# Optimization experiments

Hardware: AMD Instinct MI355X
Metric: run time of the kernel (lower is better)

The kernel has to match this reference:

```python
import math
import jax
import jax.numpy as jnp
import numpy as np

B, S, S_IMG, D, H, MAX_SEQ = 8, 1024, 1, 1024, 16, 1024
HD = D // H


def setup_inputs() -> dict:
    key = jax.random.key(0)
    ks = jax.random.split(key, 8)
    w = 0.02  # GPT-2 init scale keeps softmax well-conditioned
    return {
        "hidden_states": jax.random.normal(ks[0], (B, S, D), jnp.float32),
        "attention_mask": jnp.ones((B, 1, 1, S + S_IMG), jnp.float32),
        "image_hidden_states": jax.random.normal(ks[1], (B, S_IMG, D), jnp.float32),
        "Wc_attn": jax.random.normal(ks[2], (D, 3 * D), jnp.float32) * w,  # Conv1D: x @ W + b
        "bc_attn": jnp.zeros((3 * D,), jnp.float32),
        "Wc_proj": jax.random.normal(ks[3], (D, D), jnp.float32) * w,
        "bc_proj": jnp.zeros((D,), jnp.float32),
        "Wuk": jax.random.normal(ks[4], (D, D), jnp.float32) * w,  # nn.Linear weight: x @ W.T
        "Wuv": jax.random.normal(ks[5], (D, D), jnp.float32) * w,
    }


def _split_heads(x):
    b, s, _ = x.shape
    return x.reshape(b, s, H, HD).transpose(0, 2, 1, 3)  # [B,H,S,hd]


def reference(hidden_states, attention_mask, image_hidden_states,
              Wc_attn, bc_attn, Wc_proj, bc_proj, Wuk, Wuv):
    # c_attn (Conv1D): x @ W + b, then split into q,k,v
    qkv = hidden_states @ Wc_attn + bc_attn
    q, k, v = jnp.split(qkv, 3, axis=-1)
    q, k, v = _split_heads(q), _split_heads(k), _split_heads(v)

    # image KV via bias-free Linear layers, appended to text KV (layer_past=None)
    k_img = _split_heads(image_hidden_states @ Wuk.T)
    v_img = _split_heads(image_hidden_states @ Wuv.T)
    k = jnp.concatenate([k, k_img], axis=2)
    v = jnp.concatenate([v, v_img], axis=2)

    Q, K = q.shape[2], k.shape[2]
    scores = jnp.einsum("bhqd,bhkd->bhqk", q, k) / math.sqrt(HD)

    # causal mask: tril(ones(max_seq_len, max_seq_len+1)) sliced to [Q,K]
    causal = jnp.tril(jnp.ones((MAX_SEQ, MAX_SEQ + 1), bool))[None, None, :Q, :K]
    scores = jnp.where(causal, scores, jnp.float32(-1e9))
    scores = jnp.where(attention_mask == 0, jnp.float32(-1e4), scores)

    p_attn = jax.nn.softmax(scores, axis=-1)  # dropout p=0 -> identity
    x = jnp.einsum("bhqk,bhkd->bhqd", p_attn, v)
    x = x.transpose(0, 2, 1, 3).reshape(hidden_states.shape[0], Q, D)
    return x @ Wc_proj + bc_proj
```

## Files before the change

kernel.cpp:

```cpp
#include <hip/hip_runtime.h>


#define DEVINL __device__ __forceinline__

typedef __attribute__((ext_vector_type(8))) short bf16x8;
typedef __attribute__((ext_vector_type(4))) float f32x4;
typedef __attribute__((ext_vector_type(16))) float f32x16;
typedef __attribute__((ext_vector_type(4))) unsigned int u32x4;

DEVINL unsigned short f2bf(float f) {
  unsigned u = __float_as_uint(f);
  u += 0x7fffu + ((u >> 16) & 1u);
  return (unsigned short)(u >> 16);
}

DEVINL void gload_lds16(const void* g, void* l) {
  __builtin_amdgcn_global_load_lds(
      (const __attribute__((address_space(1))) void*)g,
      (__attribute__((address_space(3))) void*)l, 16, 0, 0);
}

#define BARRIER() asm volatile("s_barrier" ::: "memory")

__global__ void cast_f32_bf16(const float* __restrict__ in,
                              unsigned short* __restrict__ out, int n4) {
  int i = blockIdx.x * blockDim.x + threadIdx.x;
  if (i >= n4) return;
  float4 f = ((const float4*)in)[i];
  uint2 o;
  o.x = (unsigned)f2bf(f.x) | ((unsigned)f2bf(f.y) << 16);
  o.y = (unsigned)f2bf(f.z) | ((unsigned)f2bf(f.w) << 16);
  ((uint2*)out)[i] = o;
}

__global__ void transpose_cast(const float* __restrict__ in,
                               unsigned short* __restrict__ out,
                               int rows, int cols) {
  __shared__ unsigned short tile[32][33];
  int bx = blockIdx.x * 32, by = blockIdx.y * 32;
  int tx = threadIdx.x, ty = threadIdx.y;
#pragma unroll
  for (int i = 0; i < 32; i += 8)
    tile[ty + i][tx] = f2bf(in[(size_t)(by + ty + i) * cols + bx + tx]);
  __syncthreads();
#pragma unroll
  for (int i = 0; i < 32; i += 8)
    out[(size_t)(bx + ty + i) * rows + by + tx] = tile[tx][ty + i];
}

DEVINL void stage_tile(const unsigned short* __restrict__ A,
                       const unsigned short* __restrict__ Bt, int m0, int n0,
                       int kt, int buf, int t, int w, unsigned char* lds) {
  const int base = buf * 24576;
#pragma unroll
  for (int i = 0; i < 2; i++) {
    const int idx = i * 256 + t;
    const int r = idx >> 2, p = idx & 3;
    const int c = p ^ ((r >> 1) & 3);
    gload_lds16(A + (size_t)(m0 + r) * 1024 + kt * 32 + c * 8,
                lds + base + (i * 256 + w * 64) * 16);
  }
#pragma unroll
  for (int i = 0; i < 4; i++) {
    const int idx = i * 256 + t;
    const int r = idx >> 2, p = idx & 3;
    const int c = p ^ ((r >> 1) & 3);
    gload_lds16(Bt + (size_t)(n0 + r) * 1024 + kt * 32 + c * 8,
                lds + base + 8192 + (i * 256 + w * 64) * 16);
  }
}

DEVINL bf16x8 readA2(const unsigned char* lds, int buf, int m, int wr, int lr,
                     int lg) {
  const int row = wr * 64 + m * 16 + lr;
  const int off = (lg ^ ((row >> 1) & 3)) << 4;
  return *(const bf16x8*)(lds + buf * 24576 + row * 64 + off);
}
DEVINL bf16x8 readB2(const unsigned char* lds, int buf, int n, int wc, int lr,
                     int lg) {
  const int row = wc * 128 + n * 16 + lr;
  const int off = (lg ^ ((row >> 1) & 3)) << 4;
  return *(const bf16x8*)(lds + buf * 24576 + 8192 + row * 64 + off);
}

DEVINL void gemm_core(const unsigned short* __restrict__ A,
                      const unsigned short* __restrict__ Bt, int m0, int n0,
                      unsigned char* lds, f32x4 (&acc)[4][8]) {
  const int t = threadIdx.x, w = t >> 6, l = t & 63, lr = l & 15, lg = l >> 4;
  const int wr = w >> 1, wc = w & 1;
  const int NT = 32;

  stage_tile(A, Bt, m0, n0, 0, 0, t, w, lds);
  stage_tile(A, Bt, m0, n0, 1, 1, t, w, lds);
  asm volatile("s_waitcnt vmcnt(6)" ::: "memory");
  __builtin_amdgcn_sched_barrier(0);
  BARRIER();

#pragma unroll 1
  for (int j = 0; j < NT; ++j) {
    const int buf = j % 3;
    if (j + 2 < NT) stage_tile(A, Bt, m0, n0, j + 2, (j + 2) % 3, t, w, lds);
    bf16x8 af[4], bf[8];
#pragma unroll
    for (int m = 0; m < 4; m++) af[m] = readA2(lds, buf, m, wr, lr, lg);
#pragma unroll
    for (int n = 0; n < 8; n++) bf[n] = readB2(lds, buf, n, wc, lr, lg);
    __builtin_amdgcn_s_setprio(1);
#pragma unroll
    for (int m = 0; m < 4; m++)
#pragma unroll
      for (int n = 0; n < 8; n++)
        acc[m][n] = __builtin_amdgcn_mfma_f32_16x16x32_bf16(af[m], bf[n],
                                                            acc[m][n], 0, 0, 0);
    __builtin_amdgcn_s_setprio(0);
    if (j + 1 < NT) {
      if (j + 2 < NT) {
        asm volatile("s_waitcnt vmcnt(6)" ::: "memory");
      } else {
        asm volatile("s_waitcnt vmcnt(0)" ::: "memory");
      }
      __builtin_amdgcn_sched_barrier(0);
      BARRIER();
    }
  }
}

DEVINL void tile_coords(int& m0, int& n0) {
  const int x = blockIdx.x & 7;
  const int local = blockIdx.x >> 3;
  const int mi = local & 7, ni = local >> 3;
  m0 = (x * 8 + mi) * 128;
  n0 = ni * 256;
}

DEVINL int perm16(int x) { return (x & 3) | ((x & 4) << 1) | ((x & 8) >> 1); }

__global__ __launch_bounds__(256, 2) void gemm_qkv(
    const unsigned short* __restrict__ A, const unsigned short* __restrict__ Bt,
    const float* __restrict__ bias, unsigned short* __restrict__ Qb,
    unsigned short* __restrict__ Kb, unsigned short* __restrict__ VTb) {
  __shared__ __align__(16) unsigned char lds[73728];
  f32x4 acc[4][8];
#pragma unroll
  for (int m = 0; m < 4; m++)
#pragma unroll
    for (int n = 0; n < 8; n++)
#pragma unroll
      for (int e = 0; e < 4; e++) acc[m][n][e] = 0.f;
  int m0, n0;
  tile_coords(m0, n0);
  gemm_core(A, Bt, m0, n0, lds, acc);

  const int t = threadIdx.x, w = t >> 6, l = t & 63, lr = l & 15, lg = l >> 4;
  const int wr = w >> 1, wc = w & 1;
  const int region = n0 >> 10;
  const int h0 = (n0 & 1023) >> 6;

  __syncthreads();
  unsigned short* epi = (unsigned short*)lds;
  if (region < 2) {
#pragma unroll
    for (int n = 0; n < 8; n++) {
      const int c = wc * 128 + n * 16 + lr;
      const float bv = bias[n0 + c];
#pragma unroll
      for (int m = 0; m < 4; m++)
#pragma unroll
        for (int e = 0; e < 4; e++) {
          const int r = wr * 64 + m * 16 + lg * 4 + e;
          epi[r * 264 + c] = f2bf(acc[m][n][e] + bv);
        }
    }
  } else {
#pragma unroll
    for (int n = 0; n < 8; n++) {
      const int c = wc * 128 + n * 16 + lr;
      const float bv = bias[n0 + c];
#pragma unroll
      for (int m = 0; m < 4; m++)
#pragma unroll
        for (int e = 0; e < 4; e++) {
          const int rp = wr * 64 + m * 16 + perm16(lg * 4 + e);
          epi[c * 136 + rp] = f2bf(acc[m][n][e] + bv);
        }
    }
  }
  __syncthreads();

  if (region < 2) {
    const int row = t & 127, half = t >> 7;
    unsigned short* dbuf = (region == 0) ? Qb : Kb;
    const int sg = m0 + row, b = sg >> 10, si = sg & 1023;
#pragma unroll
    for (int hh = 0; hh < 2; hh++) {
      const int head = h0 + half * 2 + hh;
      const unsigned short* src = epi + row * 264 + half * 128 + hh * 64;
      unsigned short* dst = dbuf + (((size_t)b * 16 + head) * 1024 + si) * 64;
#pragma unroll
      for (int i = 0; i < 8; i++)
        ((u32x4*)dst)[i] = *(const u32x4*)(src + i * 8);
    }
  } else {
    const int c = t;
    const int head = h0 + (c >> 6), hd = c & 63;
    const int b = m0 >> 10, s0 = m0 & 1023;
    const unsigned short* src = epi + c * 136;
    unsigned short* dst = VTb + (((size_t)b * 16 + head) * 64 + hd) * 1024 + s0;
#pragma unroll
    for (int i = 0; i < 16; i++)
      ((u32x4*)dst)[i] = *(const u32x4*)(src + i * 8);
  }
}

__global__ __launch_bounds__(256, 2) void gemm_proj(
    const unsigned short* __restrict__ A, const unsigned short* __restrict__ Bt,
    const float* __restrict__ bias, float* __restrict__ out) {
  __shared__ __align__(16) unsigned char lds[73728];
  f32x4 acc[4][8];
#pragma unroll
  for (int m = 0; m < 4; m++)
#pragma unroll
    for (int n = 0; n < 8; n++)
#pragma unroll
      for (int e = 0; e < 4; e++) acc[m][n][e] = 0.f;
  int m0, n0;
  tile_coords(m0, n0);
  gemm_core(A, Bt, m0, n0, lds, acc);
  const int t = threadIdx.x, w = t >> 6, l = t & 63, lr = l & 15, lg = l >> 4;
  const int wr = w >> 1, wc = w & 1;
#pragma unroll
  for (int n = 0; n < 8; n++) {
    const int col = n0 + wc * 128 + n * 16 + lr;
    const float bv = bias[col];
#pragma unroll
    for (int m = 0; m < 4; m++)
#pragma unroll
      for (int e = 0; e < 4; e++) {
        const int row = m0 + wr * 64 + m * 16 + lg * 4 + e;
        out[(size_t)row * 1024 + col] = acc[m][n][e] + bv;
      }
  }
}

DEVINL void load_kv(int j0, const unsigned short* kbase,
                    const unsigned short* vb0, const unsigned short* vb1,
                    bf16x8 (&kf)[4], bf16x8 (&vf)[4]) {
#pragma unroll
  for (int ks = 0; ks < 4; ks++)
    kf[ks] = *(const bf16x8*)(kbase + (size_t)j0 * 64 + ks * 16);
  vf[0] = *(const bf16x8*)(vb0 + j0);
  vf[1] = *(const bf16x8*)(vb0 + j0 + 16);
  vf[2] = *(const bf16x8*)(vb1 + j0);
  vf[3] = *(const bf16x8*)(vb1 + j0 + 16);
}

template <bool DIAG>
DEVINL void attn_group(int r, int hi, const bf16x8 (&kf)[4],
                       const bf16x8 (&vf)[4], const bf16x8 (&qf)[4],
                       f32x16& o0, f32x16& o1, float& lsum) {
  f32x16 s;
#pragma unroll
  for (int e = 0; e < 16; e++) s[e] = 0.f;
  __builtin_amdgcn_s_setprio(1);
#pragma unroll
  for (int ks = 0; ks < 4; ks++)
    s = __builtin_amdgcn_mfma_f32_32x32x16_bf16(kf[ks], qf[ks], s, 0, 0, 0);
  __builtin_amdgcn_s_setprio(0);
  float p[16];
  float ls = 0.f;
#pragma unroll
  for (int e = 0; e < 16; e++) {
    float pv = __expf(s[e] * 0.125f);
    if (DIAG) {
      const int jr = (e & 3) + 8 * (e >> 2) + 4 * hi;
      if (jr > r) pv = 0.f;
    }
    p[e] = pv;
    ls += pv;
  }
  lsum += ls;
  unsigned wv[8];
#pragma unroll
  for (int i = 0; i < 8; i++)
    asm("v_cvt_pk_bf16_f32 %0, %1, %2"
        : "=v"(wv[i]) : "v"(p[2 * i]), "v"(p[2 * i + 1]));
  u32x4 w0, w1;
  w0[0] = wv[0]; w0[1] = wv[1]; w0[2] = wv[2]; w0[3] = wv[3];
  w1[0] = wv[4]; w1[1] = wv[5]; w1[2] = wv[6]; w1[3] = wv[7];
  bf16x8 pa0 = __builtin_bit_cast(bf16x8, w0);
  bf16x8 pa1 = __builtin_bit_cast(bf16x8, w1);
  __builtin_amdgcn_s_setprio(1);
  o0 = __builtin_amdgcn_mfma_f32_32x32x16_bf16(pa0, vf[0], o0, 0, 0, 0);
  o0 = __builtin_amdgcn_mfma_f32_32x32x16_bf16(pa1, vf[1], o0, 0, 0, 0);
  o1 = __builtin_amdgcn_mfma_f32_32x32x16_bf16(pa0, vf[2], o1, 0, 0, 0);
  o1 = __builtin_amdgcn_mfma_f32_32x32x16_bf16(pa1, vf[3], o1, 0, 0, 0);
  __builtin_amdgcn_s_setprio(0);
}

__global__ __launch_bounds__(256) void attn_kernel(
    const unsigned short* __restrict__ Qb, const unsigned short* __restrict__ Kb,
    const unsigned short* __restrict__ VTb, unsigned short* __restrict__ Xb) {
  __shared__ float lsums[4][2][32];
  const int bh = blockIdx.x;
  const int t = threadIdx.x, w = t >> 6, l = t & 63;
  const int r = l & 31, hi = l >> 5;
  const int qbase = blockIdx.y * 256 + w * 64;

  bf16x8 qfA[4], qfB[4];
  const unsigned short* qp = Qb + ((size_t)bh * 1024 + qbase + r) * 64 + hi * 8;
#pragma unroll
  for (int ks = 0; ks < 4; ks++) {
    qfA[ks] = *(const bf16x8*)(qp + ks * 16);
    qfB[ks] = *(const bf16x8*)(qp + 32 * 64 + ks * 16);
  }

  f32x16 oA0, oA1, oB0, oB1;
#pragma unroll
  for (int e = 0; e < 16; e++) {
    oA0[e] = 0.f; oA1[e] = 0.f; oB0[e] = 0.f; oB1[e] = 0.f;
  }
  float lsumA = 0.f, lsumB = 0.f;

  const unsigned short* kbase = Kb + ((size_t)bh * 1024 + r) * 64 + hi * 8;
  const unsigned short* vb0 = VTb + ((size_t)(bh * 64 + r)) * 1024 + hi * 8;
  const unsigned short* vb1 = vb0 + (size_t)32 * 1024;
  const int nd = qbase >> 5;

  bf16x8 kf[4], vf[4];
  load_kv(0, kbase, vb0, vb1, kf, vf);
#pragma unroll 1
  for (int tt = 0; tt < nd; ++tt) {
    bf16x8 kn[4], vn[4];
    load_kv((tt + 1) * 32, kbase, vb0, vb1, kn, vn);
    attn_group<false>(r, hi, kf, vf, qfA, oA0, oA1, lsumA);
    attn_group<false>(r, hi, kf, vf, qfB, oB0, oB1, lsumB);
#pragma unroll
    for (int i = 0; i < 4; i++) { kf[i] = kn[i]; vf[i] = vn[i]; }
  }
  {
    bf16x8 kn[4], vn[4];
    load_kv((nd + 1) * 32, kbase, vb0, vb1, kn, vn);
    attn_group<true>(r, hi, kf, vf, qfA, oA0, oA1, lsumA);
    attn_group<false>(r, hi, kf, vf, qfB, oB0, oB1, lsumB);
#pragma unroll
    for (int i = 0; i < 4; i++) { kf[i] = kn[i]; vf[i] = vn[i]; }
  }
  attn_group<true>(r, hi, kf, vf, qfB, oB0, oB1, lsumB);

  float ltotA = lsumA + __shfl_xor(lsumA, 32, 64);
  float ltotB = lsumB + __shfl_xor(lsumB, 32, 64);
  if (l < 32) { lsums[w][0][l] = ltotA; lsums[w][1][l] = ltotB; }

  const int bb = bh >> 4, h = bh & 15;
#pragma unroll
  for (int e = 0; e < 16; e++) {
    const int rw = (e & 3) + 8 * (e >> 2) + 4 * hi;
    const float invA = 1.0f / lsums[w][0][rw];
    const float invB = 1.0f / lsums[w][1][rw];
    unsigned short* xpA =
        Xb + ((size_t)bb * 1024 + qbase + rw) * 1024 + h * 64 + r;
    unsigned short* xpB = xpA + (size_t)32 * 1024;
    xpA[0]  = f2bf(oA0[e] * invA);
    xpA[32] = f2bf(oA1[e] * invA);
    xpB[0]  = f2bf(oB0[e] * invB);
    xpB[32] = f2bf(oB1[e] * invB);
  }
}

extern "C" void kernel_launch(void* const* d_in, const int* in_sizes, int n_in,
                              void* d_out, int out_size, void* d_ws,
                              size_t ws_size, hipStream_t stream) {
  const float* hidden = (const float*)d_in[0];
  const float* Wattn = (const float*)d_in[3];
  const float* battn = (const float*)d_in[4];
  const float* Wproj = (const float*)d_in[5];
  const float* bproj = (const float*)d_in[6];

  unsigned short* hB  = (unsigned short*)d_ws;
  unsigned short* WaT = hB + (size_t)8192 * 1024;
  unsigned short* WpT = WaT + (size_t)3072 * 1024;
  unsigned short* Qb  = WpT + (size_t)1024 * 1024;
  unsigned short* Kb  = Qb + (size_t)8192 * 1024;
  unsigned short* VTb = Kb + (size_t)8192 * 1024;
  unsigned short* Xb  = hB;

  cast_f32_bf16<<<8192, 256, 0, stream>>>(hidden, hB, 2097152);
  transpose_cast<<<dim3(96, 32), dim3(32, 8), 0, stream>>>(Wattn, WaT, 1024, 3072);
  transpose_cast<<<dim3(32, 32), dim3(32, 8), 0, stream>>>(Wproj, WpT, 1024, 1024);
  gemm_qkv<<<768, 256, 0, stream>>>(hB, WaT, battn, Qb, Kb, VTb);
  attn_kernel<<<dim3(128, 4), 256, 0, stream>>>(Qb, Kb, VTb, Xb);
  gemm_proj<<<256, 256, 0, stream>>>(Xb, WpT, bproj, (float*)d_out);
}
```

Measured before the change: 158.7 us.

## Split GEMM k-step into two MFMA phases interleaving B reads and staging

The shared GEMM main loop is restructured so each k-step runs in two halves. Each half loads only four B fragments from LDS and issues part of the next tile's global-to-LDS copies: A in the first half, B in the second. Barriers and explicit lgkmcnt waits are placed around each MFMA block. The aim is to overlap LDS reads and memory issue with matrix math and to cut fragment register pressure, at the cost of extra barriers per iteration.

```diff
diff --git a/kernel.cpp b/kernel.cpp
--- a/kernel.cpp
+++ b/kernel.cpp
@@ -21,6 +21,11 @@
 }
 
 #define BARRIER() asm volatile("s_barrier" ::: "memory")
+#define LGKM0()                                           \
+  do {                                                    \
+    asm volatile("s_waitcnt lgkmcnt(0)" ::: "memory");    \
+    __builtin_amdgcn_sched_barrier(0);                    \
+  } while (0)
 
 __global__ void cast_f32_bf16(const float* __restrict__ in,
                               unsigned short* __restrict__ out, int n4) {
@@ -48,9 +53,9 @@
     out[(size_t)(bx + ty + i) * rows + by + tx] = tile[tx][ty + i];
 }
 
-DEVINL void stage_tile(const unsigned short* __restrict__ A,
-                       const unsigned short* __restrict__ Bt, int m0, int n0,
-                       int kt, int buf, int t, int w, unsigned char* lds) {
+
+DEVINL void stage_a(const unsigned short* __restrict__ A, int m0, int kt,
+                    int buf, int t, int w, unsigned char* lds) {
   const int base = buf * 24576;
 #pragma unroll
   for (int i = 0; i < 2; i++) {
@@ -60,13 +65,17 @@
     gload_lds16(A + (size_t)(m0 + r) * 1024 + kt * 32 + c * 8,
                 lds + base + (i * 256 + w * 64) * 16);
   }
+}
+DEVINL void stage_b(const unsigned short* __restrict__ Bt, int n0, int kt,
+                    int buf, int t, int w, unsigned char* lds) {
+  const int base = buf * 24576 + 8192;
 #pragma unroll
   for (int i = 0; i < 4; i++) {
     const int idx = i * 256 + t;
     const int r = idx >> 2, p = idx & 3;
     const int c = p ^ ((r >> 1) & 3);
     gload_lds16(Bt + (size_t)(n0 + r) * 1024 + kt * 32 + c * 8,
-                lds + base + 8192 + (i * 256 + w * 64) * 16);
+                lds + base + (i * 256 + w * 64) * 16);
   }
 }
 
@@ -90,29 +99,37 @@
   const int wr = w >> 1, wc = w & 1;
   const int NT = 32;
 
-  stage_tile(A, Bt, m0, n0, 0, 0, t, w, lds);
-  stage_tile(A, Bt, m0, n0, 1, 1, t, w, lds);
+  stage_a(A, m0, 0, 0, t, w, lds);
+  stage_b(Bt, n0, 0, 0, t, w, lds);
+  stage_a(A, m0, 1, 1, t, w, lds);
+  stage_b(Bt, n0, 1, 1, t, w, lds);
   asm volatile("s_waitcnt vmcnt(6)" ::: "memory");
   __builtin_amdgcn_sched_barrier(0);
   BARRIER();
 
 #pragma unroll 1
   for (int j = 0; j < NT; ++j) {
-    const int buf = j % 3;
-    if (j + 2 < NT) stage_tile(A, Bt, m0, n0, j + 2, (j + 2) % 3, t, w, lds);
-    bf16x8 af[4], bf[8];
+    const int buf = j % 3, nbuf = (j + 2) % 3;
+    bf16x8 af[4], bf[4];
 #pragma unroll
     for (int m = 0; m < 4; m++) af[m] = readA2(lds, buf, m, wr, lr, lg);
 #pragma unroll
-    for (int n = 0; n < 8; n++) bf[n] = readB2(lds, buf, n, wc, lr, lg);
+    for (int n = 0; n < 4; n++) bf[n] = readB2(lds, buf, n, wc, lr, lg);
+    if (j + 2 < NT) stage_a(A, m0, j + 2, nbuf, t, w, lds);
+    BARRIER();
+    LGKM0();
     __builtin_amdgcn_s_setprio(1);
 #pragma unroll
     for (int m = 0; m < 4; m++)
 #pragma unroll
-      for (int n = 0; n < 8; n++)
+      for (int n = 0; n < 4; n++)
         acc[m][n] = __builtin_amdgcn_mfma_f32_16x16x32_bf16(af[m], bf[n],
                                                             acc[m][n], 0, 0, 0);
     __builtin_amdgcn_s_setprio(0);
+    BARRIER();
+#pragma unroll
+    for (int n = 0; n < 4; n++) bf[n] = readB2(lds, buf, n + 4, wc, lr, lg);
+    if (j + 2 < NT) stage_b(Bt, n0, j + 2, nbuf, t, w, lds);
     if (j + 1 < NT) {
       if (j + 2 < NT) {
         asm volatile("s_waitcnt vmcnt(6)" ::: "memory");
@@ -120,8 +137,18 @@
         asm volatile("s_waitcnt vmcnt(0)" ::: "memory");
       }
       __builtin_amdgcn_sched_barrier(0);
-      BARRIER();
     }
+    BARRIER();
+    LGKM0();
+    __builtin_amdgcn_s_setprio(1);
+#pragma unroll
+    for (int m = 0; m < 4; m++)
+#pragma unroll
+      for (int n = 0; n < 4; n++)
+        acc[m][n + 4] = __builtin_amdgcn_mfma_f32_16x16x32_bf16(
+            af[m], bf[n], acc[m][n + 4], 0, 0, 0);
+    __builtin_amdgcn_s_setprio(0);
+    if (j + 1 < NT) BARRIER();
   }
 }
 
```

Measured after the change: 159.2 us. Within noise of the previous version (+0.3%).
